# Performance work log

Hardware: AMD Instinct MI355X
Metric: run time of the kernel (lower is better)

The kernel has to match this reference:

```python
import jax, jax.numpy as jnp
import numpy as np

B, S, H, NH = 2, 2048, 2048, 16
HD = H // NH  # 128


def setup_inputs() -> dict:
    key = jax.random.key(0)
    ks = jax.random.split(key, 10)
    scale = 0.02
    hidden_states = jax.random.normal(ks[0], (B, S, H), dtype=jnp.float32)
    # additive causal mask [1,1,S,S]
    causal = jnp.tril(jnp.ones((S, S), dtype=jnp.bool_))
    attention_mask = jnp.where(causal, 0.0, -1e9).astype(jnp.float32)[None, None]
    def lin(k):
        kw, kb = jax.random.split(k)
        return (jax.random.normal(kw, (H, H), dtype=jnp.float32) * scale,
                jnp.zeros((H,), dtype=jnp.float32))
    Wq, bq = lin(ks[1])
    Wk, bk = lin(ks[2])
    Wv, bv = lin(ks[3])
    Wo, bo = lin(ks[4])
    return {"hidden_states": hidden_states, "attention_mask": attention_mask,
            "Wq": Wq, "bq": bq, "Wk": Wk, "bk": bk, "Wv": Wv, "bv": bv,
            "Wo": Wo, "bo": bo}


def reference(hidden_states, attention_mask, Wq, bq, Wk, bk, Wv, bv, Wo, bo):
    b, s, h = hidden_states.shape
    def shape(t):  # [b,s,h] -> [b,nh,s,hd]
        return t.reshape(b, s, NH, HD).transpose(0, 2, 1, 3)
    q = shape(hidden_states @ Wq.T + bq)
    k = shape(hidden_states @ Wk.T + bk)
    v = shape(hidden_states @ Wv.T + bv)
    attn = jnp.einsum('bnqd,bnkd->bnqk', q, k) / jnp.sqrt(jnp.float32(HD))
    attn = attn + attention_mask
    attn = jax.nn.softmax(attn, axis=-1)
    out = jnp.einsum('bnqk,bnkd->bnqd', attn, v)
    out = out.transpose(0, 2, 1, 3).reshape(b, s, h)
    return out @ Wo.T + bo
```

## Files before the change

### kernel.cpp

```cpp
#include <hip/hip_runtime.h>
#include <hip/hip_bf16.h>

#define SEQ   2048
#define HDIM  2048
#define NHEAD 16
#define HEADD 128
#define BATCH 2
#define MTOT  (BATCH*SEQ)
#define BH    (BATCH*NHEAD)

typedef __attribute__((ext_vector_type(8))) __bf16 bf16x8;
typedef __attribute__((ext_vector_type(4))) float f32x4;
typedef __attribute__((ext_vector_type(16))) float f32x16;
typedef __attribute__((ext_vector_type(8))) unsigned short u16x8;

__device__ __forceinline__ unsigned short f2b(float f) {
    __bf16 h = (__bf16)f;
    return __builtin_bit_cast(unsigned short, h);
}

__device__ __forceinline__ void gld_lds16(const void* gptr, void* ldsptr) {
    __builtin_amdgcn_global_load_lds(
        (const __attribute__((address_space(1))) unsigned int*)gptr,
        (__attribute__((address_space(3))) unsigned int*)ldsptr,
        16, 0, 0);
}

__global__ void cvt_bf16(const float* __restrict__ src, unsigned short* __restrict__ dst, long n8) {
    long i = blockIdx.x * (long)blockDim.x + threadIdx.x;
    long stride = (long)gridDim.x * blockDim.x;
    for (; i < n8; i += stride) {
        f32x4 a = *(const f32x4*)(src + i * 8);
        f32x4 b = *(const f32x4*)(src + i * 8 + 4);
        u16x8 o;
#pragma unroll
        for (int j = 0; j < 4; ++j) { o[j] = f2b(a[j]); o[4 + j] = f2b(b[j]); }
        *(u16x8*)(dst + i * 8) = o;
    }
}

__global__ void cvt5(const float* __restrict__ s0, const float* __restrict__ s1,
                     const float* __restrict__ s2, const float* __restrict__ s3,
                     const float* __restrict__ s4,
                     unsigned short* __restrict__ d0, unsigned short* __restrict__ d1,
                     unsigned short* __restrict__ d2, unsigned short* __restrict__ d3,
                     unsigned short* __restrict__ d4,
                     long n0, long n1) {
    const float* s; unsigned short* d; long n;
    switch (blockIdx.z) {
        case 0: s = s0; d = d0; n = n0; break;
        case 1: s = s1; d = d1; n = n1; break;
        case 2: s = s2; d = d2; n = n1; break;
        case 3: s = s3; d = d3; n = n1; break;
        default: s = s4; d = d4; n = n1; break;
    }
    long i = blockIdx.x * (long)blockDim.x + threadIdx.x;
    long stride = (long)gridDim.x * blockDim.x;
    for (; i < n; i += stride) {
        f32x4 a = *(const f32x4*)(s + i * 8);
        f32x4 b = *(const f32x4*)(s + i * 8 + 4);
        u16x8 o;
#pragma unroll
        for (int j = 0; j < 4; ++j) { o[j] = f2b(a[j]); o[4 + j] = f2b(b[j]); }
        *(u16x8*)(d + i * 8) = o;
    }
}

template <int MODE>
__launch_bounds__(256)
__global__ void gemm_bt(const unsigned short* __restrict__ A,
                        const unsigned short* __restrict__ Bw,
                        const float* __restrict__ bias,
                        void* __restrict__ Cout,
                        int Kc, float scale) {
    __shared__ unsigned short As[128 * 32];
    __shared__ unsigned short Bs[128 * 32];
    const int tid  = threadIdx.x;
    const int lane = tid & 63;
    const int w    = tid >> 6;

    const int wgid = blockIdx.y * gridDim.x + blockIdx.x;
    const int cpx  = (gridDim.x * gridDim.y) >> 3;
    const int swz  = (wgid & 7) * cpx + (wgid >> 3);
    const int m0 = (swz % gridDim.x) * 128, n0 = (swz / gridDim.x) * 128;

    const int wr = (w >> 1) * 64, wc = (w & 1) * 64;
    const long rowBytes = (long)Kc * 2;

    f32x4 acc[4][4] = {};

    const int kIters = Kc >> 5;
    for (int kt = 0; kt < kIters; ++kt) {
        const long kb = (long)kt * 64;
#pragma unroll
        for (int i = 0; i < 2; ++i) {
            int c = tid + i * 256;
            int row = c >> 2;
            int cb  = (c & 3) * 16;
            gld_lds16((const char*)A  + (long)(m0 + row) * rowBytes + kb + cb, (char*)As + c * 16);
            gld_lds16((const char*)Bw + (long)(n0 + row) * rowBytes + kb + cb, (char*)Bs + c * 16);
        }
        __syncthreads();
        bf16x8 af[4], bfr[4];
#pragma unroll
        for (int f = 0; f < 4; ++f) {
            af[f]  = *(const bf16x8*)&As[(wr + f * 16 + (lane & 15)) * 32 + (lane >> 4) * 8];
            bfr[f] = *(const bf16x8*)&Bs[(wc + f * 16 + (lane & 15)) * 32 + (lane >> 4) * 8];
        }
#pragma unroll
        for (int mf = 0; mf < 4; ++mf)
#pragma unroll
            for (int nf = 0; nf < 4; ++nf)
                acc[mf][nf] = __builtin_amdgcn_mfma_f32_16x16x32_bf16(af[mf], bfr[nf], acc[mf][nf], 0, 0, 0);
        __syncthreads();
    }

#pragma unroll
    for (int mf = 0; mf < 4; ++mf) {
#pragma unroll
        for (int nf = 0; nf < 4; ++nf) {
            int n = n0 + wc + nf * 16 + (lane & 15);
            float bv = bias[n];
#pragma unroll
            for (int j = 0; j < 4; ++j) {
                int m = m0 + wr + mf * 16 + (lane >> 4) * 4 + j;
                float v = (acc[mf][nf][j] + bv) * scale;
                if (MODE == 0) {
                    int b = m >> 11, s = m & 2047;
                    int nh = n >> 7, hd = n & 127;
                    ((unsigned short*)Cout)[((long)(b * NHEAD + nh) * SEQ + s) * HEADD + hd] = f2b(v);
                } else if (MODE == 1) {
                    int b = m >> 11, s = m & 2047;
                    int nh = n >> 7, hd = n & 127;
                    ((unsigned short*)Cout)[((long)(b * NHEAD + nh) * HEADD + hd) * SEQ + s] = f2b(v);
                } else {
                    ((float*)Cout)[(long)m * HDIM + n] = v;
                }
            }
        }
    }
}


__device__ __forceinline__ void attn_step32(
    const unsigned short* Ksb, const unsigned short* Vsb, char* Psw,
    const bf16x8 (&qf)[8], f32x16 (&acc)[4], float& mrun, float& lrun,
    int lane, int q0w, int kvt, bool diag)
{
    const int ql = lane & 31;
    const int hi = lane >> 5;

    f32x16 sv[2];
#pragma unroll
    for (int kvb = 0; kvb < 2; ++kvb) {
        f32x16 s = {};
        const int row = kvb * 32 + ql;
        const int sw  = (row & 7) << 4;
#pragma unroll
        for (int kc = 0; kc < 8; ++kc) {
            int off = (row * 256 + ((kc * 32 + hi * 16) ^ sw)) >> 1;
            bf16x8 kf = *(const bf16x8*)&Ksb[off];
            s = __builtin_amdgcn_mfma_f32_32x32x16_bf16(kf, qf[kc], s, 0, 0, 0);
        }
        sv[kvb] = s;
    }

    if (diag) {
        const int qg = q0w + ql;
#pragma unroll
        for (int kvb = 0; kvb < 2; ++kvb)
#pragma unroll
            for (int r = 0; r < 16; ++r) {
                int kv = kvt * 64 + kvb * 32 + (r & 3) + 8 * (r >> 2) + 4 * hi;
                if (kv > qg) sv[kvb][r] = -1e30f;
            }
    }

    float tmax = sv[0][0];
#pragma unroll
    for (int kvb = 0; kvb < 2; ++kvb)
#pragma unroll
        for (int r = 0; r < 16; ++r) tmax = fmaxf(tmax, sv[kvb][r]);
    tmax = fmaxf(tmax, __shfl_xor(tmax, 32));

    float mnew = mrun, sc = 1.0f;
    if (__any(tmax > mrun + 8.0f)) {
        mnew = fmaxf(mrun, tmax);
        sc = __expf(mrun - mnew);
#pragma unroll
        for (int db = 0; db < 4; ++db) acc[db] *= sc;
    }
    float rs = 0.f;
#pragma unroll
    for (int kvb = 0; kvb < 2; ++kvb)
#pragma unroll
        for (int r = 0; r < 16; ++r) {
            float p = __expf(sv[kvb][r] - mnew);
            sv[kvb][r] = p;
            rs += p;
        }
    rs += __shfl_xor(rs, 32);
    lrun = lrun * sc + rs;
    mrun = mnew;

#pragma unroll
    for (int kvb = 0; kvb < 2; ++kvb)
#pragma unroll
        for (int m = 0; m < 4; ++m) {
            unsigned int w0 = f2b(sv[kvb][m * 4 + 0]) | ((unsigned int)f2b(sv[kvb][m * 4 + 1]) << 16);
            unsigned int w1 = f2b(sv[kvb][m * 4 + 2]) | ((unsigned int)f2b(sv[kvb][m * 4 + 3]) << 16);
            int off = ql * 128 + ((kvb * 64 + m * 16 + hi * 8) ^ ((ql & 7) << 4));
            *(unsigned long long*)(Psw + off) =
                (unsigned long long)w0 | ((unsigned long long)w1 << 32);
        }
    bf16x8 pf[4];
#pragma unroll
    for (int kc2 = 0; kc2 < 4; ++kc2) {
        int off = ql * 128 + ((kc2 * 32 + hi * 16) ^ ((ql & 7) << 4));
        pf[kc2] = *(const bf16x8*)(Psw + off);
    }

#pragma unroll
    for (int db = 0; db < 4; ++db) {
        const int row = db * 32 + ql;
        const int sw  = (row & 7) << 4;
#pragma unroll
        for (int kc2 = 0; kc2 < 4; ++kc2) {
            int off = (row * 128 + ((kc2 * 32 + hi * 16) ^ sw)) >> 1;
            bf16x8 vf = *(const bf16x8*)&Vsb[off];
            acc[db] = __builtin_amdgcn_mfma_f32_32x32x16_bf16(vf, pf[kc2], acc[db], 0, 0, 0);
        }
    }
}

__device__ __forceinline__ void attn_epilogue(
    const f32x16 (&acc)[4], float lrun, char* Psw,
    unsigned short* __restrict__ Out, int b, int nh, int q0w, int lane)
{
    const int ql = lane & 31, hi = lane >> 5;
    const float inv = 1.0f / lrun;
#pragma unroll
    for (int db = 0; db < 4; ++db)
#pragma unroll
        for (int m = 0; m < 4; ++m) {
            unsigned int w0 = f2b(acc[db][m * 4 + 0] * inv) | ((unsigned int)f2b(acc[db][m * 4 + 1] * inv) << 16);
            unsigned int w1 = f2b(acc[db][m * 4 + 2] * inv) | ((unsigned int)f2b(acc[db][m * 4 + 3] * inv) << 16);
            int off = ql * 256 + ((db * 64 + m * 16 + hi * 8) ^ ((ql & 7) << 4));
            *(unsigned long long*)(Psw + off) =
                (unsigned long long)w0 | ((unsigned long long)w1 << 32);
        }
    __syncthreads();
#pragma unroll
    for (int it = 0; it < 8; ++it) {
        int row = it * 4 + (lane >> 4);
        int sub = lane & 15;
        int off = row * 256 + ((sub * 16) ^ ((row & 7) << 4));
        *(u16x8*)(Out + ((long)(b * SEQ) + q0w + row) * HDIM + nh * HEADD + sub * 8) =
            *(const u16x8*)(Psw + off);
    }
}

__launch_bounds__(256)
__global__ void attn_fwd(const unsigned short* __restrict__ Q,
                         const unsigned short* __restrict__ K,
                         const unsigned short* __restrict__ Vt,
                         unsigned short* __restrict__ Out) {
    __shared__ unsigned short Ks[2][64 * 128];
    __shared__ unsigned short Vs[2][128 * 64];
    __shared__ unsigned short Ps[4][4096];

    const int tid  = threadIdx.x;
    const int lane = tid & 63;
    const int w    = tid >> 6;

    const int id  = blockIdx.x;
    const int xcd = id & 7;
    const int j   = id >> 3;
    const int bh  = xcd * 4 + (j >> 3);
    const int x   = j & 7;
    const int hiT = 15 - x;
    const int loT = x;
    const int nA  = 2 * hiT + 2;
    const int nB  = 2 * loT + 2;
    const int q0A = hiT * 128 + w * 32;
    const int q0B = loT * 128 + w * 32;

    const char* Kbase = (const char*)(K  + (long)bh * SEQ * HEADD);
    const char* Vbase = (const char*)(Vt + (long)bh * HEADD * SEQ);
    char* Psw = (char*)&Ps[w][0];

    bf16x8 qfA[8], qfB[8];
#pragma unroll
    for (int kc = 0; kc < 8; ++kc) {
        qfA[kc] = *(const bf16x8*)&Q[((long)bh * SEQ + q0A + (lane & 31)) * HEADD + kc * 16 + (lane >> 5) * 8];
        qfB[kc] = *(const bf16x8*)&Q[((long)bh * SEQ + q0B + (lane & 31)) * HEADD + kc * 16 + (lane >> 5) * 8];
    }

#define STAGE(kvt, b) do {                                                              \
    _Pragma("unroll")                                                                   \
    for (int i = 0; i < 4; ++i) {                                                       \
        int c = tid + i * 256;                                                          \
        int rowk = c >> 4;                                                              \
        int cbk  = ((c & 15) * 16) ^ ((rowk & 7) << 4);                                 \
        gld_lds16(Kbase + (long)((kvt) * 64 + rowk) * 256 + cbk, (char*)Ks[b] + c * 16);\
        int rowv = c >> 3;                                                              \
        int cbv  = ((c & 7) * 16) ^ ((rowv & 7) << 4);                                  \
        gld_lds16(Vbase + (long)rowv * (SEQ * 2) + (kvt) * 128 + cbv, (char*)Vs[b] + c * 16); \
    } } while (0)

    const int b = bh >> 4, nh = bh & 15;
    int buf = 0;

    STAGE(0, 0);
    __syncthreads();

    {
        f32x16 acc[4] = {};
        float mrun = -1e30f, lrun = 0.f;
        for (int s = 0; s < nA; ++s) {
            if (s + 1 < nA) STAGE(s + 1, buf ^ 1);
            else            STAGE(0, buf ^ 1);
            attn_step32(Ks[buf], Vs[buf], Psw, qfA, acc, mrun, lrun,
                        lane, q0A, s, s * 64 + 63 > q0A);
            __syncthreads();
            buf ^= 1;
        }
        attn_epilogue(acc, lrun, Psw, Out, b, nh, q0A, lane);
    }

    {
        f32x16 acc[4] = {};
        float mrun = -1e30f, lrun = 0.f;
        for (int s = 0; s < nB; ++s) {
            if (s + 1 < nB) STAGE(s + 1, buf ^ 1);
            attn_step32(Ks[buf], Vs[buf], Psw, qfB, acc, mrun, lrun,
                        lane, q0B, s, s * 64 + 63 > q0B);
            __syncthreads();
            buf ^= 1;
        }
        attn_epilogue(acc, lrun, Psw, Out, b, nh, q0B, lane);
    }
#undef STAGE
}

extern "C" void kernel_launch(void* const* d_in, const int* in_sizes, int n_in,
                              void* d_out, int out_size, void* d_ws, size_t ws_size,
                              hipStream_t stream) {
    const float* hs = (const float*)d_in[0];
    const float* Wq = (const float*)d_in[2];
    const float* bq = (const float*)d_in[3];
    const float* Wk = (const float*)d_in[4];
    const float* bk = (const float*)d_in[5];
    const float* Wv = (const float*)d_in[6];
    const float* bv = (const float*)d_in[7];
    const float* Wo = (const float*)d_in[8];
    const float* bo = (const float*)d_in[9];
    float* out = (float*)d_out;

    char* ws = (char*)d_ws;
    const long MB = 1024L * 1024L;
    const float rs = 0.08838834764831845f;
    dim3 gg(MTOT / 128, HDIM / 128);

    if (ws_size >= 96 * MB) {
        unsigned short* hsb = (unsigned short*)ws;
        unsigned short* wqb = (unsigned short*)(ws + 16 * MB);
        unsigned short* wkb = (unsigned short*)(ws + 24 * MB);
        unsigned short* wvb = (unsigned short*)(ws + 32 * MB);
        unsigned short* wob = (unsigned short*)(ws + 40 * MB);
        unsigned short* qb  = (unsigned short*)(ws + 48 * MB);
        unsigned short* kb  = (unsigned short*)(ws + 64 * MB);
        unsigned short* vtb = (unsigned short*)(ws + 80 * MB);
        unsigned short* aob = hsb;

        cvt5<<<dim3(1024, 1, 5), 256, 0, stream>>>(hs, Wq, Wk, Wv, Wo,
                                                   hsb, wqb, wkb, wvb, wob,
                                                   (long)MTOT * HDIM / 8, (long)HDIM * HDIM / 8);
        gemm_bt<0><<<gg, 256, 0, stream>>>(hsb, wqb, bq, qb,  HDIM, rs);
        gemm_bt<0><<<gg, 256, 0, stream>>>(hsb, wkb, bk, kb,  HDIM, 1.0f);
        gemm_bt<1><<<gg, 256, 0, stream>>>(hsb, wvb, bv, vtb, HDIM, 1.0f);
        attn_fwd<<<256, 256, 0, stream>>>(qb, kb, vtb, aob);
        gemm_bt<2><<<gg, 256, 0, stream>>>(aob, wob, bo, out, HDIM, 1.0f);
    } else {
        unsigned short* hsb = (unsigned short*)ws;
        unsigned short* wb  = (unsigned short*)(ws + 16 * MB);
        unsigned short* qb  = (unsigned short*)(ws + 24 * MB);
        unsigned short* kb  = (unsigned short*)(ws + 40 * MB);
        unsigned short* vtb = (unsigned short*)(ws + 56 * MB);
        unsigned short* aob = hsb;

        cvt_bf16<<<2048, 256, 0, stream>>>(hs, hsb, (long)MTOT * HDIM / 8);
        cvt_bf16<<<2048, 256, 0, stream>>>(Wq, wb, (long)HDIM * HDIM / 8);
        gemm_bt<0><<<gg, 256, 0, stream>>>(hsb, wb, bq, qb, HDIM, rs);
        cvt_bf16<<<2048, 256, 0, stream>>>(Wk, wb, (long)HDIM * HDIM / 8);
        gemm_bt<0><<<gg, 256, 0, stream>>>(hsb, wb, bk, kb, HDIM, 1.0f);
        cvt_bf16<<<2048, 256, 0, stream>>>(Wv, wb, (long)HDIM * HDIM / 8);
        gemm_bt<1><<<gg, 256, 0, stream>>>(hsb, wb, bv, vtb, HDIM, 1.0f);
        attn_fwd<<<256, 256, 0, stream>>>(qb, kb, vtb, aob);
        cvt_bf16<<<2048, 256, 0, stream>>>(Wo, wb, (long)HDIM * HDIM / 8);
        gemm_bt<2><<<gg, 256, 0, stream>>>(aob, wb, bo, out, HDIM, 1.0f);
    }
}
```

Before: 326.4 us.

## Fuse QKV projections into one triple-buffered 256x128 GEMM kernel

Adds a new 512-thread GEMM kernel with a 256x128 output tile and a three-stage LDS ring fed by direct global-to-LDS loads. The LDS layout is XOR-swizzled, and waits are explicit vmcnt/barrier calls so that loads for later K tiles overlap the MFMA work. The Q, K and V weights are packed contiguously so a single launch computes all three projections, picking bias, scale and output layout per N range; the output projection uses the same kernel. The aim is to cut launch count, raise MFMA utilisation and hide global-load latency. The cost is about 144KB of LDS per block, which limits occupancy to one block per CU. The fallback path also changes the attention grid and drops the old tile swizzle.

```diff
diff --git a/kernel.cpp b/kernel.cpp
--- a/kernel.cpp
+++ b/kernel.cpp
@@ -67,6 +67,135 @@
 }
 
 template <int MODE>
+__launch_bounds__(512)
+__global__ void gemm256(const unsigned short* __restrict__ A,
+                        const unsigned short* __restrict__ Bw,
+                        const float* __restrict__ b0, const float* __restrict__ b1,
+                        const float* __restrict__ b2,
+                        void* __restrict__ Cout, float rs) {
+    __shared__ unsigned short Abuf[3][256 * 64];
+    __shared__ unsigned short Bbuf[3][128 * 64];
+
+    const int tid  = threadIdx.x;
+    const int lane = tid & 63;
+    const int w    = tid >> 6;
+    const int wr   = w >> 2;
+    const int wc   = w & 3;
+
+    const int nwg = gridDim.x;
+    const int cpx = nwg >> 3;
+    const int swz = (blockIdx.x & 7) * cpx + (blockIdx.x >> 3);
+    const int m0  = (swz & 15) * 256;
+    const int n0g = (swz >> 4) * 128;
+    const long rowB = (long)HDIM * 2;
+
+    const char* Ab = (const char*)A  + (long)m0  * rowB;
+    const char* Bb = (const char*)Bw + (long)n0g * rowB;
+
+#define GSTAGE(kt, bi) do {                                                      \
+    _Pragma("unroll")                                                            \
+    for (int i = 0; i < 4; ++i) {                                                \
+        int c = tid + i * 512; int row = c >> 3, slot = c & 7;                   \
+        int sc = (slot * 16) ^ ((row & 7) << 4);                                 \
+        gld_lds16(Ab + (long)row * rowB + (kt) * 128 + sc, (char*)Abuf[bi] + c * 16); \
+    }                                                                            \
+    _Pragma("unroll")                                                            \
+    for (int i = 0; i < 2; ++i) {                                                \
+        int c = tid + i * 512; int row = c >> 3, slot = c & 7;                   \
+        int sc = (slot * 16) ^ ((row & 7) << 4);                                 \
+        gld_lds16(Bb + (long)row * rowB + (kt) * 128 + sc, (char*)Bbuf[bi] + c * 16); \
+    } } while (0)
+
+    f32x4 acc[8][2] = {};
+
+    GSTAGE(0, 0);
+    GSTAGE(1, 1);
+    asm volatile("s_waitcnt vmcnt(6)" ::: "memory");
+    __builtin_amdgcn_s_barrier();
+
+    const int NT = HDIM / 64;
+    int cur = 0;
+    for (int t = 0; t < NT; ++t) {
+        const int nxt = (cur + 2 >= 3) ? cur - 1 : cur + 2;
+        if (t + 2 < NT) GSTAGE(t + 2, nxt);
+
+        const unsigned short* As = Abuf[cur];
+        const unsigned short* Bs = Bbuf[cur];
+#pragma unroll
+        for (int ks = 0; ks < 2; ++ks) {
+            bf16x8 af[8], bfr[2];
+#pragma unroll
+            for (int mf = 0; mf < 8; ++mf) {
+                int row = wr * 128 + mf * 16 + (lane & 15);
+                int off = row * 128 + ((ks * 64 + (lane >> 4) * 16) ^ ((row & 7) << 4));
+                af[mf] = *(const bf16x8*)((const char*)As + off);
+            }
+#pragma unroll
+            for (int nf = 0; nf < 2; ++nf) {
+                int row = wc * 32 + nf * 16 + (lane & 15);
+                int off = row * 128 + ((ks * 64 + (lane >> 4) * 16) ^ ((row & 7) << 4));
+                bfr[nf] = *(const bf16x8*)((const char*)Bs + off);
+            }
+            __builtin_amdgcn_s_setprio(1);
+#pragma unroll
+            for (int mf = 0; mf < 8; ++mf)
+#pragma unroll
+                for (int nf = 0; nf < 2; ++nf)
+                    acc[mf][nf] = __builtin_amdgcn_mfma_f32_16x16x32_bf16(af[mf], bfr[nf], acc[mf][nf], 0, 0, 0);
+            __builtin_amdgcn_s_setprio(0);
+        }
+
+        if (t + 2 < NT) asm volatile("s_waitcnt vmcnt(6) lgkmcnt(0)" ::: "memory");
+        else            asm volatile("s_waitcnt vmcnt(0) lgkmcnt(0)" ::: "memory");
+        __builtin_amdgcn_s_barrier();
+        cur = (cur + 1 >= 3) ? 0 : cur + 1;
+    }
+#undef GSTAGE
+
+    if (MODE == 0) {
+        const int mat = n0g >> 11;
+        const float* bb = (mat == 0) ? b0 : (mat == 1) ? b1 : b2;
+        const float scale = (mat == 0) ? rs : 1.0f;
+        unsigned short* O = (unsigned short*)Cout + (long)mat * 8388608;
+#pragma unroll
+        for (int mf = 0; mf < 8; ++mf) {
+#pragma unroll
+            for (int nf = 0; nf < 2; ++nf) {
+                int ng = n0g + wc * 32 + nf * 16 + (lane & 15);
+                int nn = ng & 2047;
+                int nh = nn >> 7, hd = nn & 127;
+                float bv = bb[nn];
+#pragma unroll
+                for (int j = 0; j < 4; ++j) {
+                    int m = m0 + wr * 128 + mf * 16 + (lane >> 4) * 4 + j;
+                    int b = m >> 11, s = m & 2047;
+                    float v = (acc[mf][nf][j] + bv) * scale;
+                    long idx;
+                    if (mat < 2) idx = ((long)(b * NHEAD + nh) * SEQ + s) * HEADD + hd;
+                    else         idx = ((long)(b * NHEAD + nh) * HEADD + hd) * SEQ + s;
+                    O[idx] = f2b(v);
+                }
+            }
+        }
+    } else {
+        float* O = (float*)Cout;
+#pragma unroll
+        for (int mf = 0; mf < 8; ++mf) {
+#pragma unroll
+            for (int nf = 0; nf < 2; ++nf) {
+                int n = n0g + wc * 32 + nf * 16 + (lane & 15);
+                float bv = b0[n];
+#pragma unroll
+                for (int j = 0; j < 4; ++j) {
+                    int m = m0 + wr * 128 + mf * 16 + (lane >> 4) * 4 + j;
+                    O[(long)m * HDIM + n] = acc[mf][nf][j] + bv;
+                }
+            }
+        }
+    }
+}
+
+template <int MODE>
 __launch_bounds__(256)
 __global__ void gemm_bt(const unsigned short* __restrict__ A,
                         const unsigned short* __restrict__ Bw,
@@ -78,17 +207,10 @@
     const int tid  = threadIdx.x;
     const int lane = tid & 63;
     const int w    = tid >> 6;
-
-    const int wgid = blockIdx.y * gridDim.x + blockIdx.x;
-    const int cpx  = (gridDim.x * gridDim.y) >> 3;
-    const int swz  = (wgid & 7) * cpx + (wgid >> 3);
-    const int m0 = (swz % gridDim.x) * 128, n0 = (swz / gridDim.x) * 128;
-
+    const int m0 = blockIdx.x * 128, n0 = blockIdx.y * 128;
     const int wr = (w >> 1) * 64, wc = (w & 1) * 64;
     const long rowBytes = (long)Kc * 2;
-
     f32x4 acc[4][4] = {};
-
     const int kIters = Kc >> 5;
     for (int kt = 0; kt < kIters; ++kt) {
         const long kb = (long)kt * 64;
@@ -114,7 +236,6 @@
                 acc[mf][nf] = __builtin_amdgcn_mfma_f32_16x16x32_bf16(af[mf], bfr[nf], acc[mf][nf], 0, 0, 0);
         __syncthreads();
     }
-
 #pragma unroll
     for (int mf = 0; mf < 4; ++mf) {
 #pragma unroll
@@ -141,7 +262,6 @@
     }
 }
 
-
 __device__ __forceinline__ void attn_step32(
     const unsigned short* Ksb, const unsigned short* Vsb, char* Psw,
     const bf16x8 (&qf)[8], f32x16 (&acc)[4], float& mrun, float& lrun,
@@ -360,27 +480,23 @@
     char* ws = (char*)d_ws;
     const long MB = 1024L * 1024L;
     const float rs = 0.08838834764831845f;
-    dim3 gg(MTOT / 128, HDIM / 128);
 
     if (ws_size >= 96 * MB) {
-        unsigned short* hsb = (unsigned short*)ws;
-        unsigned short* wqb = (unsigned short*)(ws + 16 * MB);
-        unsigned short* wkb = (unsigned short*)(ws + 24 * MB);
-        unsigned short* wvb = (unsigned short*)(ws + 32 * MB);
-        unsigned short* wob = (unsigned short*)(ws + 40 * MB);
-        unsigned short* qb  = (unsigned short*)(ws + 48 * MB);
-        unsigned short* kb  = (unsigned short*)(ws + 64 * MB);
-        unsigned short* vtb = (unsigned short*)(ws + 80 * MB);
-        unsigned short* aob = hsb;
-
-        cvt5<<<dim3(1024, 1, 5), 256, 0, stream>>>(hs, Wq, Wk, Wv, Wo,
-                                                   hsb, wqb, wkb, wvb, wob,
-                                                   (long)MTOT * HDIM / 8, (long)HDIM * HDIM / 8);
-        gemm_bt<0><<<gg, 256, 0, stream>>>(hsb, wqb, bq, qb,  HDIM, rs);
-        gemm_bt<0><<<gg, 256, 0, stream>>>(hsb, wkb, bk, kb,  HDIM, 1.0f);
-        gemm_bt<1><<<gg, 256, 0, stream>>>(hsb, wvb, bv, vtb, HDIM, 1.0f);
+        unsigned short* hsb  = (unsigned short*)ws;
+        unsigned short* wqkv = (unsigned short*)(ws + 16 * MB);
+        unsigned short* wob  = (unsigned short*)(ws + 40 * MB);
+        unsigned short* qb   = (unsigned short*)(ws + 48 * MB);
+        unsigned short* kb   = (unsigned short*)(ws + 64 * MB);
+        unsigned short* vtb  = (unsigned short*)(ws + 80 * MB);
+        unsigned short* aob  = hsb;
+
+        cvt5<<<dim3(1024, 1, 5), 256, 0, stream>>>(
+            hs, Wq, Wk, Wv, Wo,
+            hsb, wqkv, wqkv + 2048L * 2048, wqkv + 2L * 2048 * 2048, wob,
+            (long)MTOT * HDIM / 8, (long)HDIM * HDIM / 8);
+        gemm256<0><<<768, 512, 0, stream>>>(hsb, wqkv, bq, bk, bv, qb, rs);
         attn_fwd<<<256, 256, 0, stream>>>(qb, kb, vtb, aob);
-        gemm_bt<2><<<gg, 256, 0, stream>>>(aob, wob, bo, out, HDIM, 1.0f);
+        gemm256<2><<<256, 512, 0, stream>>>(aob, wob, bo, bo, bo, out, 1.0f);
     } else {
         unsigned short* hsb = (unsigned short*)ws;
         unsigned short* wb  = (unsigned short*)(ws + 16 * MB);
@@ -388,6 +504,7 @@
         unsigned short* kb  = (unsigned short*)(ws + 40 * MB);
         unsigned short* vtb = (unsigned short*)(ws + 56 * MB);
         unsigned short* aob = hsb;
+        dim3 gg(MTOT / 128, HDIM / 128);
 
         cvt_bf16<<<2048, 256, 0, stream>>>(hs, hsb, (long)MTOT * HDIM / 8);
         cvt_bf16<<<2048, 256, 0, stream>>>(Wq, wb, (long)HDIM * HDIM / 8);
@@ -396,7 +513,7 @@
         gemm_bt<0><<<gg, 256, 0, stream>>>(hsb, wb, bk, kb, HDIM, 1.0f);
         cvt_bf16<<<2048, 256, 0, stream>>>(Wv, wb, (long)HDIM * HDIM / 8);
         gemm_bt<1><<<gg, 256, 0, stream>>>(hsb, wb, bv, vtb, HDIM, 1.0f);
-        attn_fwd<<<256, 256, 0, stream>>>(qb, kb, vtb, aob);
+        attn_fwd<<<512, 256, 0, stream>>>(qb, kb, vtb, aob);
         cvt_bf16<<<2048, 256, 0, stream>>>(Wo, wb, (long)HDIM * HDIM / 8);
         gemm_bt<2><<<gg, 256, 0, stream>>>(aob, wb, bo, out, HDIM, 1.0f);
     }
```

Result: no change. 332.4 us (+1.8%).

## Split attention KV tiles across two wave groups with in-register P and merge

Applied to the files above, without the earlier changes.

The attention kernel now runs 512 threads, with two groups of four waves. Each group handles one 32-key half of every 64-key KV tile for the same query rows, and the two partial softmax states and accumulators are merged through LDS at the end. The P matrix is repacked in registers with v_permlane32_swap instead of a round trip through LDS, and s_setprio is raised around the MFMA sections. This is meant to raise wave-level parallelism and cut LDS traffic in the inner loop. The cost is extra merge synchronisation, one Q load per pass instead of holding both, and reliance on the permlane32 swap instruction.

```diff
diff --git a/kernel.cpp b/kernel.cpp
--- a/kernel.cpp
+++ b/kernel.cpp
@@ -142,45 +142,42 @@
 }
 
 
-__device__ __forceinline__ void attn_step32(
-    const unsigned short* Ksb, const unsigned short* Vsb, char* Psw,
+#define MASKV (-3.0e38f)
+
+__device__ __forceinline__ void attn_step32s(
+    const unsigned short* Ksb, const unsigned short* Vsb,
     const bf16x8 (&qf)[8], f32x16 (&acc)[4], float& mrun, float& lrun,
-    int lane, int q0w, int kvt, bool diag)
+    int lane, int p, int q0w, int kvt, bool diag)
 {
     const int ql = lane & 31;
     const int hi = lane >> 5;
 
-    f32x16 sv[2];
-#pragma unroll
-    for (int kvb = 0; kvb < 2; ++kvb) {
-        f32x16 s = {};
-        const int row = kvb * 32 + ql;
+    f32x16 sv = {};
+    {
+        const int row = p * 32 + ql;
         const int sw  = (row & 7) << 4;
+        __builtin_amdgcn_s_setprio(1);
 #pragma unroll
         for (int kc = 0; kc < 8; ++kc) {
             int off = (row * 256 + ((kc * 32 + hi * 16) ^ sw)) >> 1;
             bf16x8 kf = *(const bf16x8*)&Ksb[off];
-            s = __builtin_amdgcn_mfma_f32_32x32x16_bf16(kf, qf[kc], s, 0, 0, 0);
-        }
-        sv[kvb] = s;
+            sv = __builtin_amdgcn_mfma_f32_32x32x16_bf16(kf, qf[kc], sv, 0, 0, 0);
+        }
+        __builtin_amdgcn_s_setprio(0);
     }
 
     if (diag) {
         const int qg = q0w + ql;
 #pragma unroll
-        for (int kvb = 0; kvb < 2; ++kvb)
-#pragma unroll
-            for (int r = 0; r < 16; ++r) {
-                int kv = kvt * 64 + kvb * 32 + (r & 3) + 8 * (r >> 2) + 4 * hi;
-                if (kv > qg) sv[kvb][r] = -1e30f;
-            }
-    }
-
-    float tmax = sv[0][0];
-#pragma unroll
-    for (int kvb = 0; kvb < 2; ++kvb)
-#pragma unroll
-        for (int r = 0; r < 16; ++r) tmax = fmaxf(tmax, sv[kvb][r]);
+        for (int r = 0; r < 16; ++r) {
+            int kv = kvt * 64 + p * 32 + (r & 3) + 8 * (r >> 2) + 4 * hi;
+            if (kv > qg) sv[r] = MASKV;
+        }
+    }
+
+    float tmax = sv[0];
+#pragma unroll
+    for (int r = 1; r < 16; ++r) tmax = fmaxf(tmax, sv[r]);
     tmax = fmaxf(tmax, __shfl_xor(tmax, 32));
 
     float mnew = mrun, sc = 1.0f;
@@ -190,88 +187,101 @@
 #pragma unroll
         for (int db = 0; db < 4; ++db) acc[db] *= sc;
     }
-    float rs = 0.f;
-#pragma unroll
-    for (int kvb = 0; kvb < 2; ++kvb)
-#pragma unroll
-        for (int r = 0; r < 16; ++r) {
-            float p = __expf(sv[kvb][r] - mnew);
-            sv[kvb][r] = p;
-            rs += p;
-        }
-    rs += __shfl_xor(rs, 32);
-    lrun = lrun * sc + rs;
+    float rsum = 0.f;
+#pragma unroll
+    for (int r = 0; r < 16; ++r) {
+        float pv = __expf(sv[r] - mnew);
+        sv[r] = pv;
+        rsum += pv;
+    }
+    rsum += __shfl_xor(rsum, 32);
+    lrun = lrun * sc + rsum;
     mrun = mnew;
 
-#pragma unroll
-    for (int kvb = 0; kvb < 2; ++kvb)
-#pragma unroll
-        for (int m = 0; m < 4; ++m) {
-            unsigned int w0 = f2b(sv[kvb][m * 4 + 0]) | ((unsigned int)f2b(sv[kvb][m * 4 + 1]) << 16);
-            unsigned int w1 = f2b(sv[kvb][m * 4 + 2]) | ((unsigned int)f2b(sv[kvb][m * 4 + 3]) << 16);
-            int off = ql * 128 + ((kvb * 64 + m * 16 + hi * 8) ^ ((ql & 7) << 4));
-            *(unsigned long long*)(Psw + off) =
-                (unsigned long long)w0 | ((unsigned long long)w1 << 32);
-        }
-    bf16x8 pf[4];
-#pragma unroll
-    for (int kc2 = 0; kc2 < 4; ++kc2) {
-        int off = ql * 128 + ((kc2 * 32 + hi * 16) ^ ((ql & 7) << 4));
-        pf[kc2] = *(const bf16x8*)(Psw + off);
-    }
-
+    bf16x8 pf[2];
+#pragma unroll
+    for (int kc2 = 0; kc2 < 2; ++kc2) {
+        unsigned int w01 = f2b(sv[8 * kc2 + 0]) | ((unsigned int)f2b(sv[8 * kc2 + 1]) << 16);
+        unsigned int w23 = f2b(sv[8 * kc2 + 2]) | ((unsigned int)f2b(sv[8 * kc2 + 3]) << 16);
+        unsigned int w45 = f2b(sv[8 * kc2 + 4]) | ((unsigned int)f2b(sv[8 * kc2 + 5]) << 16);
+        unsigned int w67 = f2b(sv[8 * kc2 + 6]) | ((unsigned int)f2b(sv[8 * kc2 + 7]) << 16);
+        asm volatile("v_permlane32_swap_b32 %0, %1" : "+v"(w01), "+v"(w45));
+        asm volatile("v_permlane32_swap_b32 %0, %1" : "+v"(w23), "+v"(w67));
+        union { unsigned int u[4]; bf16x8 v; } pk;
+        pk.u[0] = w01; pk.u[1] = w23; pk.u[2] = w45; pk.u[3] = w67;
+        pf[kc2] = pk.v;
+    }
+
+    __builtin_amdgcn_s_setprio(1);
 #pragma unroll
     for (int db = 0; db < 4; ++db) {
         const int row = db * 32 + ql;
         const int sw  = (row & 7) << 4;
 #pragma unroll
-        for (int kc2 = 0; kc2 < 4; ++kc2) {
-            int off = (row * 128 + ((kc2 * 32 + hi * 16) ^ sw)) >> 1;
+        for (int kc2 = 0; kc2 < 2; ++kc2) {
+            int off = (row * 128 + ((p * 64 + kc2 * 32 + hi * 16) ^ sw)) >> 1;
             bf16x8 vf = *(const bf16x8*)&Vsb[off];
             acc[db] = __builtin_amdgcn_mfma_f32_32x32x16_bf16(vf, pf[kc2], acc[db], 0, 0, 0);
         }
     }
-}
-
-__device__ __forceinline__ void attn_epilogue(
-    const f32x16 (&acc)[4], float lrun, char* Psw,
-    unsigned short* __restrict__ Out, int b, int nh, int q0w, int lane)
+    __builtin_amdgcn_s_setprio(0);
+}
+
+__device__ __forceinline__ void attn_merge_store(
+    f32x16 (&acc)[4], float mrun, float lrun,
+    float (*Mx)[32], float (*Lx)[32], f32x16 (*Ob)[64],
+    unsigned short* __restrict__ Out, long rowbase, int lane, int wp, int p)
 {
     const int ql = lane & 31, hi = lane >> 5;
-    const float inv = 1.0f / lrun;
-#pragma unroll
-    for (int db = 0; db < 4; ++db)
-#pragma unroll
-        for (int m = 0; m < 4; ++m) {
-            unsigned int w0 = f2b(acc[db][m * 4 + 0] * inv) | ((unsigned int)f2b(acc[db][m * 4 + 1] * inv) << 16);
-            unsigned int w1 = f2b(acc[db][m * 4 + 2] * inv) | ((unsigned int)f2b(acc[db][m * 4 + 3] * inv) << 16);
-            int off = ql * 256 + ((db * 64 + m * 16 + hi * 8) ^ ((ql & 7) << 4));
-            *(unsigned long long*)(Psw + off) =
-                (unsigned long long)w0 | ((unsigned long long)w1 << 32);
-        }
+    Mx[wp * 2 + p][ql] = mrun;
+    Lx[wp * 2 + p][ql] = lrun;
     __syncthreads();
-#pragma unroll
-    for (int it = 0; it < 8; ++it) {
-        int row = it * 4 + (lane >> 4);
-        int sub = lane & 15;
-        int off = row * 256 + ((sub * 16) ^ ((row & 7) << 4));
-        *(u16x8*)(Out + ((long)(b * SEQ) + q0w + row) * HDIM + nh * HEADD + sub * 8) =
-            *(const u16x8*)(Psw + off);
-    }
-}
-
-__launch_bounds__(256)
+    const float mo = Mx[wp * 2 + 1 - p][ql];
+    const float lo = Lx[wp * 2 + 1 - p][ql];
+    const float M  = fmaxf(mrun, mo);
+    const float a  = __expf(mrun - M);
+    const float L  = lrun * a + lo * __expf(mo - M);
+#pragma unroll
+    for (int db = 0; db < 4; ++db) acc[db] *= a;
+#pragma unroll
+    for (int db = 0; db < 4; ++db) {
+        if (p == 1) Ob[wp][lane] = acc[db];
+        __syncthreads();
+        if (p == 0) acc[db] += Ob[wp][lane];
+        __syncthreads();
+    }
+    if (p == 0) {
+        const float inv = 1.0f / L;
+        const long base = rowbase + (long)ql * HDIM;
+#pragma unroll
+        for (int db = 0; db < 4; ++db)
+#pragma unroll
+            for (int mm = 0; mm < 4; ++mm) {
+                int d0 = db * 32 + 8 * mm + 4 * hi;
+                unsigned int w0 = f2b(acc[db][4 * mm + 0] * inv) | ((unsigned int)f2b(acc[db][4 * mm + 1] * inv) << 16);
+                unsigned int w1 = f2b(acc[db][4 * mm + 2] * inv) | ((unsigned int)f2b(acc[db][4 * mm + 3] * inv) << 16);
+                *(unsigned long long*)(Out + base + d0) =
+                    (unsigned long long)w0 | ((unsigned long long)w1 << 32);
+            }
+    }
+}
+
+__launch_bounds__(512, 1)
 __global__ void attn_fwd(const unsigned short* __restrict__ Q,
                          const unsigned short* __restrict__ K,
                          const unsigned short* __restrict__ Vt,
                          unsigned short* __restrict__ Out) {
     __shared__ unsigned short Ks[2][64 * 128];
     __shared__ unsigned short Vs[2][128 * 64];
-    __shared__ unsigned short Ps[4][4096];
+    __shared__ float Mx[8][32];
+    __shared__ float Lx[8][32];
+    __shared__ f32x16 Ob[4][64];
 
     const int tid  = threadIdx.x;
     const int lane = tid & 63;
     const int w    = tid >> 6;
+    const int wp   = w & 3;
+    const int p    = w >> 2;
 
     const int id  = blockIdx.x;
     const int xcd = id & 7;
@@ -282,30 +292,22 @@
     const int loT = x;
     const int nA  = 2 * hiT + 2;
     const int nB  = 2 * loT + 2;
-    const int q0A = hiT * 128 + w * 32;
-    const int q0B = loT * 128 + w * 32;
+    const int q0A = hiT * 128 + wp * 32;
+    const int q0B = loT * 128 + wp * 32;
 
     const char* Kbase = (const char*)(K  + (long)bh * SEQ * HEADD);
     const char* Vbase = (const char*)(Vt + (long)bh * HEADD * SEQ);
-    char* Psw = (char*)&Ps[w][0];
-
-    bf16x8 qfA[8], qfB[8];
-#pragma unroll
-    for (int kc = 0; kc < 8; ++kc) {
-        qfA[kc] = *(const bf16x8*)&Q[((long)bh * SEQ + q0A + (lane & 31)) * HEADD + kc * 16 + (lane >> 5) * 8];
-        qfB[kc] = *(const bf16x8*)&Q[((long)bh * SEQ + q0B + (lane & 31)) * HEADD + kc * 16 + (lane >> 5) * 8];
-    }
-
-#define STAGE(kvt, b) do {                                                              \
+
+#define STAGE(kvt, bb) do {                                                             \
     _Pragma("unroll")                                                                   \
-    for (int i = 0; i < 4; ++i) {                                                       \
-        int c = tid + i * 256;                                                          \
+    for (int i = 0; i < 2; ++i) {                                                       \
+        int c = tid + i * 512;                                                          \
         int rowk = c >> 4;                                                              \
         int cbk  = ((c & 15) * 16) ^ ((rowk & 7) << 4);                                 \
-        gld_lds16(Kbase + (long)((kvt) * 64 + rowk) * 256 + cbk, (char*)Ks[b] + c * 16);\
+        gld_lds16(Kbase + (long)((kvt) * 64 + rowk) * 256 + cbk, (char*)Ks[bb] + c * 16);\
         int rowv = c >> 3;                                                              \
         int cbv  = ((c & 7) * 16) ^ ((rowv & 7) << 4);                                  \
-        gld_lds16(Vbase + (long)rowv * (SEQ * 2) + (kvt) * 128 + cbv, (char*)Vs[b] + c * 16); \
+        gld_lds16(Vbase + (long)rowv * (SEQ * 2) + (kvt) * 128 + cbv, (char*)Vs[bb] + c * 16); \
     } } while (0)
 
     const int b = bh >> 4, nh = bh & 15;
@@ -315,30 +317,42 @@
     __syncthreads();
 
     {
+        bf16x8 qf[8];
+#pragma unroll
+        for (int kc = 0; kc < 8; ++kc)
+            qf[kc] = *(const bf16x8*)&Q[((long)bh * SEQ + q0A + (lane & 31)) * HEADD + kc * 16 + (lane >> 5) * 8];
+
         f32x16 acc[4] = {};
         float mrun = -1e30f, lrun = 0.f;
         for (int s = 0; s < nA; ++s) {
             if (s + 1 < nA) STAGE(s + 1, buf ^ 1);
             else            STAGE(0, buf ^ 1);
-            attn_step32(Ks[buf], Vs[buf], Psw, qfA, acc, mrun, lrun,
-                        lane, q0A, s, s * 64 + 63 > q0A);
+            attn_step32s(Ks[buf], Vs[buf], qf, acc, mrun, lrun,
+                         lane, p, q0A, s, s * 64 + 63 > q0A);
             __syncthreads();
             buf ^= 1;
         }
-        attn_epilogue(acc, lrun, Psw, Out, b, nh, q0A, lane);
+        attn_merge_store(acc, mrun, lrun, Mx, Lx, Ob, Out,
+                         ((long)(b * SEQ) + q0A) * HDIM + nh * HEADD, lane, wp, p);
     }
 
     {
+        bf16x8 qf[8];
+#pragma unroll
+        for (int kc = 0; kc < 8; ++kc)
+            qf[kc] = *(const bf16x8*)&Q[((long)bh * SEQ + q0B + (lane & 31)) * HEADD + kc * 16 + (lane >> 5) * 8];
+
         f32x16 acc[4] = {};
         float mrun = -1e30f, lrun = 0.f;
         for (int s = 0; s < nB; ++s) {
             if (s + 1 < nB) STAGE(s + 1, buf ^ 1);
-            attn_step32(Ks[buf], Vs[buf], Psw, qfB, acc, mrun, lrun,
-                        lane, q0B, s, s * 64 + 63 > q0B);
+            attn_step32s(Ks[buf], Vs[buf], qf, acc, mrun, lrun,
+                         lane, p, q0B, s, s * 64 + 63 > q0B);
             __syncthreads();
             buf ^= 1;
         }
-        attn_epilogue(acc, lrun, Psw, Out, b, nh, q0B, lane);
+        attn_merge_store(acc, mrun, lrun, Mx, Lx, Ob, Out,
+                         ((long)(b * SEQ) + q0B) * HDIM + nh * HEADD, lane, wp, p);
     }
 #undef STAGE
 }
@@ -363,23 +377,25 @@
     dim3 gg(MTOT / 128, HDIM / 128);
 
     if (ws_size >= 96 * MB) {
-        unsigned short* hsb = (unsigned short*)ws;
-        unsigned short* wqb = (unsigned short*)(ws + 16 * MB);
-        unsigned short* wkb = (unsigned short*)(ws + 24 * MB);
-        unsigned short* wvb = (unsigned short*)(ws + 32 * MB);
-        unsigned short* wob = (unsigned short*)(ws + 40 * MB);
-        unsigned short* qb  = (unsigned short*)(ws + 48 * MB);
-        unsigned short* kb  = (unsigned short*)(ws + 64 * MB);
-        unsigned short* vtb = (unsigned short*)(ws + 80 * MB);
-        unsigned short* aob = hsb;
-
-        cvt5<<<dim3(1024, 1, 5), 256, 0, stream>>>(hs, Wq, Wk, Wv, Wo,
-                                                   hsb, wqb, wkb, wvb, wob,
-                                                   (long)MTOT * HDIM / 8, (long)HDIM * HDIM / 8);
+        unsigned short* hsb  = (unsigned short*)ws;
+        unsigned short* wqkv = (unsigned short*)(ws + 16 * MB);
+        unsigned short* wob  = (unsigned short*)(ws + 40 * MB);
+        unsigned short* qb   = (unsigned short*)(ws + 48 * MB);
+        unsigned short* kb   = (unsigned short*)(ws + 64 * MB);
+        unsigned short* vtb  = (unsigned short*)(ws + 80 * MB);
+        unsigned short* aob  = hsb;
+        unsigned short* wqb  = wqkv;
+        unsigned short* wkb  = wqkv + 2048L * 2048;
+        unsigned short* wvb  = wqkv + 2L * 2048 * 2048;
+
+        cvt5<<<dim3(1024, 1, 5), 256, 0, stream>>>(
+            hs, Wq, Wk, Wv, Wo,
+            hsb, wqb, wkb, wvb, wob,
+            (long)MTOT * HDIM / 8, (long)HDIM * HDIM / 8);
         gemm_bt<0><<<gg, 256, 0, stream>>>(hsb, wqb, bq, qb,  HDIM, rs);
         gemm_bt<0><<<gg, 256, 0, stream>>>(hsb, wkb, bk, kb,  HDIM, 1.0f);
         gemm_bt<1><<<gg, 256, 0, stream>>>(hsb, wvb, bv, vtb, HDIM, 1.0f);
-        attn_fwd<<<256, 256, 0, stream>>>(qb, kb, vtb, aob);
+        attn_fwd<<<256, 512, 0, stream>>>(qb, kb, vtb, aob);
         gemm_bt<2><<<gg, 256, 0, stream>>>(aob, wob, bo, out, HDIM, 1.0f);
     } else {
         unsigned short* hsb = (unsigned short*)ws;
@@ -396,7 +412,7 @@
         gemm_bt<0><<<gg, 256, 0, stream>>>(hsb, wb, bk, kb, HDIM, 1.0f);
         cvt_bf16<<<2048, 256, 0, stream>>>(Wv, wb, (long)HDIM * HDIM / 8);
         gemm_bt<1><<<gg, 256, 0, stream>>>(hsb, wb, bv, vtb, HDIM, 1.0f);
-        attn_fwd<<<256, 256, 0, stream>>>(qb, kb, vtb, aob);
+        attn_fwd<<<256, 512, 0, stream>>>(qb, kb, vtb, aob);
         cvt_bf16<<<2048, 256, 0, stream>>>(Wo, wb, (long)HDIM * HDIM / 8);
         gemm_bt<2><<<gg, 256, 0, stream>>>(aob, wb, bo, out, HDIM, 1.0f);
     }
```

Measured after the change: 311.0 us. 1.05x faster.
